# Kernel tuning notes

Hardware: AMD Instinct MI355X
Metric: run time of the kernel (lower is better)

Reference implementation:

```python
import jax, jax.numpy as jnp
import numpy as np

B, Q, K, H = 8, 512, 512, 64
KEY_D, QUERY_D, VAL_D = 256, 256, 256

def setup_inputs() -> dict:
    key = jax.random.key(0)
    ks = jax.random.split(key, 6)
    return {
        "key": jax.random.normal(ks[0], (B, K, KEY_D), dtype=jnp.float32),
        "query": jax.random.normal(ks[1], (B, Q, QUERY_D), dtype=jnp.float32),
        "value": jax.random.normal(ks[2], (B, K, VAL_D), dtype=jnp.float32),
        "mask": jnp.zeros((B, Q, K), dtype=bool),
        "W_k": jax.random.normal(ks[3], (KEY_D, H), dtype=jnp.float32) / np.sqrt(KEY_D),
        "W_q": jax.random.normal(ks[4], (QUERY_D, H), dtype=jnp.float32) / np.sqrt(QUERY_D),
        "w_v": jax.random.normal(ks[5], (H,), dtype=jnp.float32) / np.sqrt(H),
    }

def reference(key, query, value, mask, W_k, W_q, w_v):
    q = query @ W_q                      # [B, Q, H]
    k = key @ W_k                        # [B, K, H]
    feats = jnp.tanh(q[:, :, None, :] + k[:, None, :, :])  # [B, Q, K, H]
    score = jnp.einsum('bqkh,h->bqk', feats, w_v)           # [B, Q, K]
    score = jnp.where(mask, -jnp.inf, score)
    attn = jax.nn.softmax(score, axis=-1)                   # [B, Q, K]
    return jnp.einsum('bqk,bkd->bqd', attn, value)          # [B, Q, VAL_D]
```

## Files before the change

kernel.cpp:

```cpp
#include <hip/hip_runtime.h>
#include <math.h>

#define NB 8
#define NQ 512
#define NK 512
#define NH 64
#define ND 256
#define QT 8

typedef float f32x2 __attribute__((ext_vector_type(2)));
typedef float f32x4 __attribute__((ext_vector_type(4)));

#define EXP2(x) __builtin_amdgcn_exp2f(x)
#define RCP(x)  __builtin_amdgcn_rcpf(x)
#define SCALE2 2.8853900817779268f
#define LOG2E  1.4426950408889634f

static __device__ __forceinline__ f32x2 sp2(float v) { return (f32x2){v, v}; }
#define FMA2(a, b, c) __builtin_elementwise_fma((a), (b), (c))

__global__ __launch_bounds__(256, 8) void proj_kernel(
    const float* __restrict__ query, const float* __restrict__ key,
    const float* __restrict__ Wq, const float* __restrict__ Wk,
    float* __restrict__ Eq, float* __restrict__ Ekp)
{
    __shared__ __align__(16) float ins[8][260];
    __shared__ float pacc[3][8][64];
    const int t = threadIdx.x;
    const bool isK = blockIdx.x >= 512;
    const float* __restrict__ in = isK ? key : query;
    const float* __restrict__ W  = isK ? Wk : Wq;
    const int rowbase = (blockIdx.x & 511) * 8;

    {
        const int r = t >> 5, c = (t & 31) * 8;
        const float* src = in + (size_t)(rowbase + r) * ND + c;
        *(f32x4*)&ins[r][c]     = *(const f32x4*)src;
        *(f32x4*)&ins[r][c + 4] = *(const f32x4*)(src + 4);
    }
    __syncthreads();

    const int lane = t & 63;
    const int w    = t >> 6;
    const int d0   = w * 64;

    float acc[8] = {0.f,0.f,0.f,0.f,0.f,0.f,0.f,0.f};
    #pragma unroll 4
    for (int dq = 0; dq < 64; dq += 4) {
        const int d = d0 + dq;
        const float w0 = W[(size_t)(d + 0) * NH + lane];
        const float w1 = W[(size_t)(d + 1) * NH + lane];
        const float w2 = W[(size_t)(d + 2) * NH + lane];
        const float w3 = W[(size_t)(d + 3) * NH + lane];
        #pragma unroll
        for (int r = 0; r < 8; ++r) {
            const f32x4 rv = *(const f32x4*)&ins[r][d];
            acc[r] = fmaf(rv.x, w0, acc[r]);
            acc[r] = fmaf(rv.y, w1, acc[r]);
            acc[r] = fmaf(rv.z, w2, acc[r]);
            acc[r] = fmaf(rv.w, w3, acc[r]);
        }
    }
    if (w > 0) {
        #pragma unroll
        for (int r = 0; r < 8; ++r) pacc[w - 1][r][lane] = acc[r];
    }
    __syncthreads();
    if (w == 0) {
        #pragma unroll
        for (int r = 0; r < 8; ++r) {
            const float a = acc[r] + pacc[0][r][lane] + pacc[1][r][lane]
                                   + pacc[2][r][lane];
            const float x = fminf(fmaxf(a * SCALE2, -30.f), 30.f);
            const float e = EXP2(x);
            const int g = rowbase + r;
            if (!isK) {
                Eq[(size_t)g * NH + lane] = e;
            } else {
                const int b = g >> 9, kk = g & 511;
                Ekp[((size_t)b * NH + lane) * NK + kk] = e;
            }
        }
    }
}

__global__ __launch_bounds__(1024, 8) void attn_kernel(
    const float* __restrict__ Eq, const float* __restrict__ Ekp,
    const float* __restrict__ value, const unsigned char* __restrict__ mask,
    const float* __restrict__ w_v, float* __restrict__ out)
{
    __shared__ __align__(16) float smA[14336];
    __shared__ __align__(16) float ps[QT][516];
    __shared__ __align__(16) float reds[QT][4];

    float* const ekb = smA;
    float* const qEq = smA + 4128;
    float* const qFq = smA + 4640;
    float* const w01 = smA + 5152;

    const int t    = threadIdx.x;
    const int lane = t & 63;
    const int ws   = t >> 6;
    const int b    = blockIdx.x >> 6;
    const int q0   = (blockIdx.x & 63) * QT;

    if (t < 512) {
        const int r = t >> 6, h = t & 63;
        const float e = Eq[(size_t)(b * NQ + q0 + r) * NH + h];
        qEq[r * 64 + h] = e;
        qFq[r * 64 + h] = w_v[h ^ 1] * e;
    }
    if (t < 32) w01[t] = w_v[2 * t] + w_v[2 * t + 1];

    float wl = w_v[lane];
    #pragma unroll
    for (int off = 32; off; off >>= 1) wl += __shfl_xor(wl, off, 64);
    const float wsumL = wl * LOG2E;

    const float* __restrict__ ekg = Ekp + (size_t)b * NH * NK;
    const int sh = t >> 8;
    const int sk = (t & 255) * 2;
    *(f32x2*)&ekb[sh * 516 + sk] = *(const f32x2*)&ekg[(size_t)sh * NK + sk];
    __syncthreads();

    const int kq4 = ws & 3;
    const int rg  = ws >> 2;
    const int kp  = kq4 * 64 + lane;
    const int r0  = 2 * rg;

    f32x2 acc0 = {0.f, 0.f}, acc1 = {0.f, 0.f};

    for (int hc = 0; hc < 16; ++hc) {
        const int buf = hc & 1;
        if (hc < 15) {
            *(f32x2*)&ekb[(buf ^ 1) * 2064 + sh * 516 + sk] =
                *(const f32x2*)&ekg[(size_t)(4 * (hc + 1) + sh) * NK + sk];
        }
        const float* Kb = &ekb[buf * 2064];
        const f32x2 ek0 = *(const f32x2*)&Kb[0 * 516 + 2 * kp];
        const f32x2 ek1 = *(const f32x2*)&Kb[1 * 516 + 2 * kp];
        const f32x2 ek2 = *(const f32x2*)&Kb[2 * 516 + 2 * kp];
        const f32x2 ek3 = *(const f32x2*)&Kb[3 * 516 + 2 * kp];
        const float w01a = w01[2 * hc], w01b = w01[2 * hc + 1];

#define SCORE4(EQV, FQV, ACCR)                                              \
        {                                                                   \
            const f32x2 t0 = ek0 * (EQV).x;                                 \
            const f32x2 t1 = ek1 * (EQV).y;                                 \
            const f32x2 ua = t0 + t1 + 1.0f;                                \
            const f32x2 dda = FMA2(t0, t1, ua);                             \
            f32x2 na = FMA2(sp2((FQV).x), ek0, sp2(w01a));                  \
            na = FMA2(sp2((FQV).y), ek1, na);                               \
            const f32x2 t2 = ek2 * (EQV).z;                                 \
            const f32x2 t3 = ek3 * (EQV).w;                                 \
            const f32x2 ub = t2 + t3 + 1.0f;                                \
            const f32x2 ddb = FMA2(t2, t3, ub);                             \
            f32x2 nb = FMA2(sp2((FQV).z), ek2, sp2(w01b));                  \
            nb = FMA2(sp2((FQV).w), ek3, nb);                               \
            const f32x2 Dv = dda * ddb;                                     \
            f32x2 Nv = na * ddb;                                            \
            Nv = FMA2(nb, dda, Nv);                                         \
            const f32x2 rD = { RCP(Dv.x), RCP(Dv.y) };                      \
            ACCR = FMA2(Nv, rD, ACCR);                                      \
        }
        {
            const f32x4 eqA = *(const f32x4*)&qEq[(r0 + 0) * 64 + 4 * hc];
            const f32x4 fqA = *(const f32x4*)&qFq[(r0 + 0) * 64 + 4 * hc];
            SCORE4(eqA, fqA, acc0);
            const f32x4 eqB = *(const f32x4*)&qEq[(r0 + 1) * 64 + 4 * hc];
            const f32x4 fqB = *(const f32x4*)&qFq[(r0 + 1) * 64 + 4 * hc];
            SCORE4(eqB, fqB, acc1);
        }
        __syncthreads();
    }

    const unsigned char* mrow0 = mask + (size_t)(b * NQ + q0 + r0) * NK + 2 * kp;
    f32x2 arg0 = FMA2(acc0, sp2(-2.f * LOG2E), sp2(wsumL));
    f32x2 arg1 = FMA2(acc1, sp2(-2.f * LOG2E), sp2(wsumL));
    const unsigned short m0 = *(const unsigned short*)mrow0;
    const unsigned short m1 = *(const unsigned short*)(mrow0 + NK);
    if (m0 & 0x00ff) arg0.x = -__builtin_inff();
    if (m0 & 0xff00) arg0.y = -__builtin_inff();
    if (m1 & 0x00ff) arg1.x = -__builtin_inff();
    if (m1 & 0xff00) arg1.y = -__builtin_inff();

    f32x2 p0 = { EXP2(arg0.x), EXP2(arg0.y) };
    f32x2 p1 = { EXP2(arg1.x), EXP2(arg1.y) };
    float h0 = p0.x + p0.y, h1 = p1.x + p1.y;
    #pragma unroll
    for (int off = 32; off; off >>= 1) {
        h0 += __shfl_xor(h0, off, 64);
        h1 += __shfl_xor(h1, off, 64);
    }
    if (lane == 0) { reds[r0][kq4] = h0; reds[r0 + 1][kq4] = h1; }
    __syncthreads();
    {
        const f32x4 s0 = *(const f32x4*)&reds[r0][0];
        const f32x4 s1 = *(const f32x4*)&reds[r0 + 1][0];
        p0 = p0 * RCP((s0.x + s0.y) + (s0.z + s0.w));
        p1 = p1 * RCP((s1.x + s1.y) + (s1.z + s1.w));
    }
    *(f32x2*)&ps[r0][2 * kp]     = p0;
    *(f32x2*)&ps[r0 + 1][2 * kp] = p1;
    __syncthreads();

    const int kq   = ws >> 1;
    const int dh   = ws & 1;
    const int dcol = dh * 128 + 2 * lane;
    f32x2 a[QT];
    #pragma unroll
    for (int r = 0; r < QT; ++r) a[r] = (f32x2){0.f, 0.f};

    const float* __restrict__ vb = value + ((size_t)b * NK + kq * 64) * ND + dcol;
    for (int kk = 0; kk < 64; kk += 2) {
        f32x2 pr[QT];
        #pragma unroll
        for (int r = 0; r < QT; ++r)
            pr[r] = *(const f32x2*)&ps[r][kq * 64 + kk];
        const f32x2 v0 = *(const f32x2*)&vb[(size_t)kk * ND];
        const f32x2 v1 = *(const f32x2*)&vb[(size_t)(kk + 1) * ND];
        #pragma unroll
        for (int r = 0; r < QT; ++r) {
            a[r] = FMA2(sp2(pr[r].x), v0, a[r]);
            a[r] = FMA2(sp2(pr[r].y), v1, a[r]);
        }
    }

    float* const pacc = smA;
    if (kq > 0) {
        #pragma unroll
        for (int r = 0; r < QT; ++r)
            *(f32x2*)&pacc[((kq - 1) * QT + r) * ND + dcol] = a[r];
    }
    __syncthreads();
    if (kq == 0) {
        #pragma unroll
        for (int r = 0; r < QT; ++r) {
            f32x2 v = a[r];
            #pragma unroll
            for (int j = 0; j < 7; ++j)
                v += *(const f32x2*)&pacc[(j * QT + r) * ND + dcol];
            *(f32x2*)&out[(size_t)(b * NQ + q0 + r) * ND + dcol] = v;
        }
    }
}

extern "C" void kernel_launch(void* const* d_in, const int* in_sizes, int n_in,
                              void* d_out, int out_size, void* d_ws, size_t ws_size,
                              hipStream_t stream) {
    const float* key   = (const float*)d_in[0];
    const float* query = (const float*)d_in[1];
    const float* value = (const float*)d_in[2];
    const unsigned char* mask = (const unsigned char*)d_in[3];
    const float* Wk  = (const float*)d_in[4];
    const float* Wq  = (const float*)d_in[5];
    const float* w_v = (const float*)d_in[6];
    float* out = (float*)d_out;

    float* Eq  = (float*)d_ws;
    float* Ekp = Eq + (size_t)NB * NQ * NH;

    proj_kernel<<<1024, 256, 0, stream>>>(query, key, Wq, Wk, Eq, Ekp);
    attn_kernel<<<NB * (NQ / QT), 1024, 0, stream>>>(Eq, Ekp, value, mask, w_v, out);
}
```

Baseline: 57.43 us.

## Restructure attention kernel to 512 threads with per-thread key and register prefetch

The attention kernel drops from 1024 to 512 threads per block. Each thread now owns one key and computes scores for all 8 queries, reading Ek values straight from global memory with a register prefetch instead of double-buffered shared memory, which removes the per-chunk barriers. The query data is repacked into a transposed interleaved shared layout so one vector load serves two queries. The value-accumulation phase uses 4 key-splits of 128 keys, and the cross-split reduction is done in two halves to shrink shared memory. The projection kernel transposes its input tile in shared memory to use packed FMAs. The cost is more registers per thread and scattered global loads of Ek.

```diff
diff --git a/kernel.cpp b/kernel.cpp
--- a/kernel.cpp
+++ b/kernel.cpp
@@ -17,15 +17,20 @@
 #define LOG2E  1.4426950408889634f
 
 static __device__ __forceinline__ f32x2 sp2(float v) { return (f32x2){v, v}; }
-#define FMA2(a, b, c) __builtin_elementwise_fma((a), (b), (c))
-
-__global__ __launch_bounds__(256, 8) void proj_kernel(
+static __device__ __forceinline__ f32x2 fma2(f32x2 a, f32x2 b, f32x2 c) {
+    return __builtin_elementwise_fma(a, b, c);
+}
+static __device__ __forceinline__ f32x2 mk2(float x, float y) {
+    return (f32x2){x, y};
+}
+
+__global__ __launch_bounds__(256, 4) void proj_kernel(
     const float* __restrict__ query, const float* __restrict__ key,
     const float* __restrict__ Wq, const float* __restrict__ Wk,
     float* __restrict__ Eq, float* __restrict__ Ekp)
 {
-    __shared__ __align__(16) float ins[8][260];
-    __shared__ float pacc[3][8][64];
+    __shared__ __align__(16) float insT[ND][12];
+    __shared__ float pacc[3][4][NH][2];
     const int t = threadIdx.x;
     const bool isK = blockIdx.x >= 512;
     const float* __restrict__ in = isK ? key : query;
@@ -33,10 +38,14 @@
     const int rowbase = (blockIdx.x & 511) * 8;
 
     {
-        const int r = t >> 5, c = (t & 31) * 8;
+        const int r = t & 7, c = (t >> 3) * 8;
         const float* src = in + (size_t)(rowbase + r) * ND + c;
-        *(f32x4*)&ins[r][c]     = *(const f32x4*)src;
-        *(f32x4*)&ins[r][c + 4] = *(const f32x4*)(src + 4);
+        const f32x4 v0 = *(const f32x4*)src;
+        const f32x4 v1 = *(const f32x4*)(src + 4);
+        insT[c + 0][r] = v0.x; insT[c + 1][r] = v0.y;
+        insT[c + 2][r] = v0.z; insT[c + 3][r] = v0.w;
+        insT[c + 4][r] = v1.x; insT[c + 5][r] = v1.y;
+        insT[c + 6][r] = v1.z; insT[c + 7][r] = v1.w;
     }
     __syncthreads();
 
@@ -44,203 +53,217 @@
     const int w    = t >> 6;
     const int d0   = w * 64;
 
-    float acc[8] = {0.f,0.f,0.f,0.f,0.f,0.f,0.f,0.f};
-    #pragma unroll 4
-    for (int dq = 0; dq < 64; dq += 4) {
-        const int d = d0 + dq;
-        const float w0 = W[(size_t)(d + 0) * NH + lane];
-        const float w1 = W[(size_t)(d + 1) * NH + lane];
-        const float w2 = W[(size_t)(d + 2) * NH + lane];
-        const float w3 = W[(size_t)(d + 3) * NH + lane];
-        #pragma unroll
-        for (int r = 0; r < 8; ++r) {
-            const f32x4 rv = *(const f32x4*)&ins[r][d];
-            acc[r] = fmaf(rv.x, w0, acc[r]);
-            acc[r] = fmaf(rv.y, w1, acc[r]);
-            acc[r] = fmaf(rv.z, w2, acc[r]);
-            acc[r] = fmaf(rv.w, w3, acc[r]);
-        }
+    f32x2 acc[4] = {{0.f,0.f},{0.f,0.f},{0.f,0.f},{0.f,0.f}};
+    for (int dd = 0; dd < 64; ++dd) {
+        const int d = d0 + dd;
+        const float wv = W[(size_t)d * NH + lane];
+        const f32x4 rA = *(const f32x4*)&insT[d][0];
+        const f32x4 rB = *(const f32x4*)&insT[d][4];
+        acc[0] = fma2(mk2(rA.x, rA.y), sp2(wv), acc[0]);
+        acc[1] = fma2(mk2(rA.z, rA.w), sp2(wv), acc[1]);
+        acc[2] = fma2(mk2(rB.x, rB.y), sp2(wv), acc[2]);
+        acc[3] = fma2(mk2(rB.z, rB.w), sp2(wv), acc[3]);
     }
     if (w > 0) {
         #pragma unroll
-        for (int r = 0; r < 8; ++r) pacc[w - 1][r][lane] = acc[r];
+        for (int rp = 0; rp < 4; ++rp)
+            *(f32x2*)&pacc[w - 1][rp][lane][0] = acc[rp];
     }
     __syncthreads();
     if (w == 0) {
-        #pragma unroll
-        for (int r = 0; r < 8; ++r) {
-            const float a = acc[r] + pacc[0][r][lane] + pacc[1][r][lane]
-                                   + pacc[2][r][lane];
-            const float x = fminf(fmaxf(a * SCALE2, -30.f), 30.f);
-            const float e = EXP2(x);
-            const int g = rowbase + r;
-            if (!isK) {
-                Eq[(size_t)g * NH + lane] = e;
-            } else {
-                const int b = g >> 9, kk = g & 511;
-                Ekp[((size_t)b * NH + lane) * NK + kk] = e;
+        float e[8];
+        #pragma unroll
+        for (int rp = 0; rp < 4; ++rp) {
+            f32x2 a = acc[rp];
+            a += *(const f32x2*)&pacc[0][rp][lane][0];
+            a += *(const f32x2*)&pacc[1][rp][lane][0];
+            a += *(const f32x2*)&pacc[2][rp][lane][0];
+            e[2 * rp] = a.x; e[2 * rp + 1] = a.y;
+        }
+        #pragma unroll
+        for (int j = 0; j < 8; ++j) {
+            const float x = fminf(fmaxf(e[j] * SCALE2, -30.f), 30.f);
+            e[j] = EXP2(x);
+        }
+        if (!isK) {
+            #pragma unroll
+            for (int j = 0; j < 8; ++j)
+                Eq[(size_t)(rowbase + j) * NH + lane] = e[j];
+        } else {
+            #pragma unroll
+            for (int j = 0; j < 8; ++j) {
+                const int g = rowbase + j;
+                const int bb = g >> 9, kk = g & 511;
+                Ekp[((size_t)bb * NH + lane) * NK + kk] = e[j];
             }
         }
     }
 }
 
-__global__ __launch_bounds__(1024, 8) void attn_kernel(
+__global__ __launch_bounds__(512, 4) void attn_kernel(
     const float* __restrict__ Eq, const float* __restrict__ Ekp,
     const float* __restrict__ value, const unsigned char* __restrict__ mask,
     const float* __restrict__ w_v, float* __restrict__ out)
 {
-    __shared__ __align__(16) float smA[14336];
-    __shared__ __align__(16) float ps[QT][516];
-    __shared__ __align__(16) float reds[QT][4];
-
-    float* const ekb = smA;
-    float* const qEq = smA + 4128;
-    float* const qFq = smA + 4640;
-    float* const w01 = smA + 5152;
+    __shared__ __align__(16) float qT[NH][4][4];
+    __shared__ float w01[32];
+    __shared__ __align__(16) float ps[QT][NK];
+    __shared__ __align__(16) float reds[QT][8];
+    __shared__ __align__(16) float pacc[3][4][ND];
 
     const int t    = threadIdx.x;
     const int lane = t & 63;
-    const int ws   = t >> 6;
+    const int w    = t >> 6;
     const int b    = blockIdx.x >> 6;
     const int q0   = (blockIdx.x & 63) * QT;
 
-    if (t < 512) {
-        const int r = t >> 6, h = t & 63;
+    {
+        const int r = w, h = lane;
         const float e = Eq[(size_t)(b * NQ + q0 + r) * NH + h];
-        qEq[r * 64 + h] = e;
-        qFq[r * 64 + h] = w_v[h ^ 1] * e;
+        qT[h][r >> 1][r & 1]       = e;
+        qT[h][r >> 1][2 + (r & 1)] = w_v[h ^ 1] * e;
     }
     if (t < 32) w01[t] = w_v[2 * t] + w_v[2 * t + 1];
-
     float wl = w_v[lane];
     #pragma unroll
     for (int off = 32; off; off >>= 1) wl += __shfl_xor(wl, off, 64);
     const float wsumL = wl * LOG2E;
-
-    const float* __restrict__ ekg = Ekp + (size_t)b * NH * NK;
-    const int sh = t >> 8;
-    const int sk = (t & 255) * 2;
-    *(f32x2*)&ekb[sh * 516 + sk] = *(const f32x2*)&ekg[(size_t)sh * NK + sk];
-    __syncthreads();
-
-    const int kq4 = ws & 3;
-    const int rg  = ws >> 2;
-    const int kp  = kq4 * 64 + lane;
-    const int r0  = 2 * rg;
-
-    f32x2 acc0 = {0.f, 0.f}, acc1 = {0.f, 0.f};
+    __syncthreads();
+
+    const int k = (w << 6) + lane;
+    const float* __restrict__ ekc = Ekp + (size_t)b * NH * NK + k;
+
+    f32x2 acc[4] = {{0.f,0.f},{0.f,0.f},{0.f,0.f},{0.f,0.f}};
+    float eka[4];
+    #pragma unroll
+    for (int j = 0; j < 4; ++j) eka[j] = ekc[(size_t)j * NK];
 
     for (int hc = 0; hc < 16; ++hc) {
-        const int buf = hc & 1;
+        const float ek0 = eka[0], ek1 = eka[1], ek2 = eka[2], ek3 = eka[3];
         if (hc < 15) {
-            *(f32x2*)&ekb[(buf ^ 1) * 2064 + sh * 516 + sk] =
-                *(const f32x2*)&ekg[(size_t)(4 * (hc + 1) + sh) * NK + sk];
-        }
-        const float* Kb = &ekb[buf * 2064];
-        const f32x2 ek0 = *(const f32x2*)&Kb[0 * 516 + 2 * kp];
-        const f32x2 ek1 = *(const f32x2*)&Kb[1 * 516 + 2 * kp];
-        const f32x2 ek2 = *(const f32x2*)&Kb[2 * 516 + 2 * kp];
-        const f32x2 ek3 = *(const f32x2*)&Kb[3 * 516 + 2 * kp];
-        const float w01a = w01[2 * hc], w01b = w01[2 * hc + 1];
-
-#define SCORE4(EQV, FQV, ACCR)                                              \
-        {                                                                   \
-            const f32x2 t0 = ek0 * (EQV).x;                                 \
-            const f32x2 t1 = ek1 * (EQV).y;                                 \
-            const f32x2 ua = t0 + t1 + 1.0f;                                \
-            const f32x2 dda = FMA2(t0, t1, ua);                             \
-            f32x2 na = FMA2(sp2((FQV).x), ek0, sp2(w01a));                  \
-            na = FMA2(sp2((FQV).y), ek1, na);                               \
-            const f32x2 t2 = ek2 * (EQV).z;                                 \
-            const f32x2 t3 = ek3 * (EQV).w;                                 \
-            const f32x2 ub = t2 + t3 + 1.0f;                                \
-            const f32x2 ddb = FMA2(t2, t3, ub);                             \
-            f32x2 nb = FMA2(sp2((FQV).z), ek2, sp2(w01b));                  \
-            nb = FMA2(sp2((FQV).w), ek3, nb);                               \
-            const f32x2 Dv = dda * ddb;                                     \
-            f32x2 Nv = na * ddb;                                            \
-            Nv = FMA2(nb, dda, Nv);                                         \
-            const f32x2 rD = { RCP(Dv.x), RCP(Dv.y) };                      \
-            ACCR = FMA2(Nv, rD, ACCR);                                      \
-        }
-        {
-            const f32x4 eqA = *(const f32x4*)&qEq[(r0 + 0) * 64 + 4 * hc];
-            const f32x4 fqA = *(const f32x4*)&qFq[(r0 + 0) * 64 + 4 * hc];
-            SCORE4(eqA, fqA, acc0);
-            const f32x4 eqB = *(const f32x4*)&qEq[(r0 + 1) * 64 + 4 * hc];
-            const f32x4 fqB = *(const f32x4*)&qFq[(r0 + 1) * 64 + 4 * hc];
-            SCORE4(eqB, fqB, acc1);
-        }
-        __syncthreads();
-    }
-
-    const unsigned char* mrow0 = mask + (size_t)(b * NQ + q0 + r0) * NK + 2 * kp;
-    f32x2 arg0 = FMA2(acc0, sp2(-2.f * LOG2E), sp2(wsumL));
-    f32x2 arg1 = FMA2(acc1, sp2(-2.f * LOG2E), sp2(wsumL));
-    const unsigned short m0 = *(const unsigned short*)mrow0;
-    const unsigned short m1 = *(const unsigned short*)(mrow0 + NK);
-    if (m0 & 0x00ff) arg0.x = -__builtin_inff();
-    if (m0 & 0xff00) arg0.y = -__builtin_inff();
-    if (m1 & 0x00ff) arg1.x = -__builtin_inff();
-    if (m1 & 0xff00) arg1.y = -__builtin_inff();
-
-    f32x2 p0 = { EXP2(arg0.x), EXP2(arg0.y) };
-    f32x2 p1 = { EXP2(arg1.x), EXP2(arg1.y) };
-    float h0 = p0.x + p0.y, h1 = p1.x + p1.y;
-    #pragma unroll
-    for (int off = 32; off; off >>= 1) {
-        h0 += __shfl_xor(h0, off, 64);
-        h1 += __shfl_xor(h1, off, 64);
-    }
-    if (lane == 0) { reds[r0][kq4] = h0; reds[r0 + 1][kq4] = h1; }
-    __syncthreads();
+            #pragma unroll
+            for (int j = 0; j < 4; ++j)
+                eka[j] = ekc[(size_t)(4 * (hc + 1) + j) * NK];
+        }
+        const f32x2 w2 = *(const f32x2*)&w01[2 * hc];
+        const int hb = 4 * hc;
+        #pragma unroll
+        for (int rp = 0; rp < 4; ++rp) {
+            const f32x4 g0 = *(const f32x4*)&qT[hb + 0][rp][0];
+            const f32x4 g1 = *(const f32x4*)&qT[hb + 1][rp][0];
+            const f32x4 g2 = *(const f32x4*)&qT[hb + 2][rp][0];
+            const f32x4 g3 = *(const f32x4*)&qT[hb + 3][rp][0];
+            const f32x2 t0 = mk2(g0.x, g0.y) * ek0;
+            const f32x2 t1 = mk2(g1.x, g1.y) * ek1;
+            const f32x2 ua = t0 + t1 + 1.0f;
+            const f32x2 da = fma2(t0, t1, ua);
+            f32x2 na = fma2(mk2(g0.z, g0.w), sp2(ek0), sp2(w2.x));
+            na = fma2(mk2(g1.z, g1.w), sp2(ek1), na);
+            const f32x2 t2 = mk2(g2.x, g2.y) * ek2;
+            const f32x2 t3 = mk2(g3.x, g3.y) * ek3;
+            const f32x2 ub = t2 + t3 + 1.0f;
+            const f32x2 db = fma2(t2, t3, ub);
+            f32x2 nb = fma2(mk2(g2.z, g2.w), sp2(ek2), sp2(w2.y));
+            nb = fma2(mk2(g3.z, g3.w), sp2(ek3), nb);
+            const f32x2 D = da * db;
+            f32x2 N = na * db;
+            N = fma2(nb, da, N);
+            const f32x2 rD = mk2(RCP(D.x), RCP(D.y));
+            acc[rp] = fma2(N, rD, acc[rp]);
+        }
+    }
+
+    float p[8];
     {
-        const f32x4 s0 = *(const f32x4*)&reds[r0][0];
-        const f32x4 s1 = *(const f32x4*)&reds[r0 + 1][0];
-        p0 = p0 * RCP((s0.x + s0.y) + (s0.z + s0.w));
-        p1 = p1 * RCP((s1.x + s1.y) + (s1.z + s1.w));
-    }
-    *(f32x2*)&ps[r0][2 * kp]     = p0;
-    *(f32x2*)&ps[r0 + 1][2 * kp] = p1;
-    __syncthreads();
-
-    const int kq   = ws >> 1;
-    const int dh   = ws & 1;
+        const unsigned char* __restrict__ mb =
+            mask + (size_t)(b * NQ + q0) * NK + k;
+        #pragma unroll
+        for (int rp = 0; rp < 4; ++rp) {
+            const f32x2 arg = fma2(acc[rp], sp2(-2.f * LOG2E), sp2(wsumL));
+            p[2 * rp]     = mb[(size_t)(2 * rp) * NK]     ? -__builtin_inff() : arg.x;
+            p[2 * rp + 1] = mb[(size_t)(2 * rp + 1) * NK] ? -__builtin_inff() : arg.y;
+        }
+        #pragma unroll
+        for (int r = 0; r < 8; ++r) p[r] = EXP2(p[r]);
+    }
+
+    #pragma unroll
+    for (int r = 0; r < 8; ++r) {
+        float s = p[r];
+        #pragma unroll
+        for (int off = 32; off; off >>= 1) s += __shfl_xor(s, off, 64);
+        if (lane == 0) reds[r][w] = s;
+    }
+    __syncthreads();
+    #pragma unroll
+    for (int r = 0; r < 8; ++r) {
+        const f32x4 sa = *(const f32x4*)&reds[r][0];
+        const f32x4 sb = *(const f32x4*)&reds[r][4];
+        const float gsum = ((sa.x + sa.y) + (sa.z + sa.w)) +
+                           ((sb.x + sb.y) + (sb.z + sb.w));
+        ps[r][k] = p[r] * RCP(gsum);
+    }
+    __syncthreads();
+
+    const int kq   = w >> 1;
+    const int dh   = w & 1;
     const int dcol = dh * 128 + 2 * lane;
     f32x2 a[QT];
     #pragma unroll
     for (int r = 0; r < QT; ++r) a[r] = (f32x2){0.f, 0.f};
 
-    const float* __restrict__ vb = value + ((size_t)b * NK + kq * 64) * ND + dcol;
-    for (int kk = 0; kk < 64; kk += 2) {
-        f32x2 pr[QT];
-        #pragma unroll
-        for (int r = 0; r < QT; ++r)
-            pr[r] = *(const f32x2*)&ps[r][kq * 64 + kk];
-        const f32x2 v0 = *(const f32x2*)&vb[(size_t)kk * ND];
+    const float* __restrict__ vb = value + ((size_t)b * NK + kq * 128) * ND + dcol;
+    for (int kk = 0; kk < 128; kk += 4) {
+        const int kbase = kq * 128 + kk;
+        const f32x2 v0 = *(const f32x2*)&vb[(size_t)(kk + 0) * ND];
         const f32x2 v1 = *(const f32x2*)&vb[(size_t)(kk + 1) * ND];
-        #pragma unroll
-        for (int r = 0; r < QT; ++r) {
-            a[r] = FMA2(sp2(pr[r].x), v0, a[r]);
-            a[r] = FMA2(sp2(pr[r].y), v1, a[r]);
-        }
-    }
-
-    float* const pacc = smA;
+        const f32x2 v2 = *(const f32x2*)&vb[(size_t)(kk + 2) * ND];
+        const f32x2 v3 = *(const f32x2*)&vb[(size_t)(kk + 3) * ND];
+        #pragma unroll
+        for (int half = 0; half < 2; ++half) {
+            #pragma unroll
+            for (int rr = 0; rr < 4; ++rr) {
+                const int r = half * 4 + rr;
+                const f32x4 P = *(const f32x4*)&ps[r][kbase];
+                a[r] = fma2(sp2(P.x), v0, a[r]);
+                a[r] = fma2(sp2(P.y), v1, a[r]);
+                a[r] = fma2(sp2(P.z), v2, a[r]);
+                a[r] = fma2(sp2(P.w), v3, a[r]);
+            }
+        }
+    }
+
     if (kq > 0) {
         #pragma unroll
-        for (int r = 0; r < QT; ++r)
-            *(f32x2*)&pacc[((kq - 1) * QT + r) * ND + dcol] = a[r];
+        for (int r = 0; r < 4; ++r)
+            *(f32x2*)&pacc[kq - 1][r][dcol] = a[r];
     }
     __syncthreads();
     if (kq == 0) {
         #pragma unroll
-        for (int r = 0; r < QT; ++r) {
+        for (int r = 0; r < 4; ++r) {
             f32x2 v = a[r];
-            #pragma unroll
-            for (int j = 0; j < 7; ++j)
-                v += *(const f32x2*)&pacc[(j * QT + r) * ND + dcol];
+            v += *(const f32x2*)&pacc[0][r][dcol];
+            v += *(const f32x2*)&pacc[1][r][dcol];
+            v += *(const f32x2*)&pacc[2][r][dcol];
             *(f32x2*)&out[(size_t)(b * NQ + q0 + r) * ND + dcol] = v;
+        }
+    }
+    __syncthreads();
+    if (kq > 0) {
+        #pragma unroll
+        for (int r = 0; r < 4; ++r)
+            *(f32x2*)&pacc[kq - 1][r][dcol] = a[4 + r];
+    }
+    __syncthreads();
+    if (kq == 0) {
+        #pragma unroll
+        for (int r = 0; r < 4; ++r) {
+            f32x2 v = a[4 + r];
+            v += *(const f32x2*)&pacc[0][r][dcol];
+            v += *(const f32x2*)&pacc[1][r][dcol];
+            v += *(const f32x2*)&pacc[2][r][dcol];
+            *(f32x2*)&out[(size_t)(b * NQ + q0 + 4 + r) * ND + dcol] = v;
         }
     }
 }
@@ -261,5 +284,5 @@
     float* Ekp = Eq + (size_t)NB * NQ * NH;
 
     proj_kernel<<<1024, 256, 0, stream>>>(query, key, Wq, Wk, Eq, Ekp);
-    attn_kernel<<<NB * (NQ / QT), 1024, 0, stream>>>(Eq, Ekp, value, mask, w_v, out);
-}
+    attn_kernel<<<NB * (NQ / QT), 512, 0, stream>>>(Eq, Ekp, value, mask, w_v, out);
+}
```

Result: faster. 48.59 us (-15.4%).
